# Kernel optimization log

Measured on AMD Instinct MI355X. Metric: run time of the kernel, lower is better.

## Reference

```python
import jax, jax.numpy as jnp
import numpy as np

D_MODEL = 1024
N_HEAD = 16
D_HEAD = D_MODEL // N_HEAD
B, S = 4, 2048


def setup_inputs() -> dict:
    key = jax.random.key(0)
    ks = jax.random.split(key, 9)
    s = 1.0 / np.sqrt(D_MODEL)
    inp = {"x": jax.random.normal(ks[0], (B, S, D_MODEL), dtype=jnp.float32)}
    for i, name in enumerate(["q", "k", "v", "o"]):
        inp[f"W{name}"] = jax.random.uniform(ks[1 + 2 * i], (D_MODEL, D_MODEL), jnp.float32, -s, s)
        inp[f"b{name}"] = jax.random.uniform(ks[2 + 2 * i], (D_MODEL,), jnp.float32, -s, s)
    return inp


def reference(x, Wq, bq, Wk, bk, Wv, bv, Wo, bo):
    b, sq, _ = x.shape
    skv = sq
    # projections (torch Linear: x @ W^T + b), reshape to (b, h, s, d)
    def proj(W, bias):
        return (x @ W.T + bias).reshape(b, sq, N_HEAD, D_HEAD).transpose(0, 2, 1, 3)
    q, k, v = proj(Wq, bq), proj(Wk, bk), proj(Wv, bv)
    scale = np.sqrt(D_HEAD).astype(np.float32)
    scores = jnp.einsum("bhqd,bhkd->bhqk", q, k) / scale
    causal_mask = jnp.triu(jnp.ones((sq, skv), dtype=bool), k=1)
    scores = jnp.where(causal_mask, -jnp.inf, scores)
    attn = jax.nn.softmax(scores, axis=-1)
    o = jnp.einsum("bhqk,bhkd->bhqd", attn, v)  # (b, h, sq, d_head)
    o = o.transpose(0, 2, 1, 3).reshape(b, sq, D_MODEL)
    return o @ Wo.T + bo
```

## Files before the change

kernel.cpp:

```cpp
#include <hip/hip_runtime.h>
#include <hip/hip_bf16.h>
#include <math.h>

#define S_LEN 2048
#define DMODEL 1024
#define NHEAD 16
#define DHEAD 64
#define BATCH 4
#define MROWS (BATCH * S_LEN)

typedef unsigned short u16;
typedef __attribute__((ext_vector_type(4))) unsigned short u16x4;
typedef __attribute__((ext_vector_type(2))) unsigned u32x2;
typedef __attribute__((ext_vector_type(8))) short bf16x8;
typedef __attribute__((ext_vector_type(4))) float f32x4;

#define GLDS16(g, l)                                              \
  __builtin_amdgcn_global_load_lds(                               \
      (const __attribute__((address_space(1))) void*)(g),         \
      (__attribute__((address_space(3))) void*)(l), 16, 0, 0)

__device__ __forceinline__ u16 f2bf(float f) {
  unsigned u = __float_as_uint(f);
  u += 0x7fff + ((u >> 16) & 1);
  return (u16)(u >> 16);
}

__device__ __forceinline__ float exp2v(float x) {
  float r;
  asm("v_exp_f32 %0, %1" : "=v"(r) : "v"(x));
  return r;
}

__device__ __forceinline__ f32x4 mfma16(bf16x8 a, bf16x8 b, f32x4 c) {
  return __builtin_amdgcn_mfma_f32_16x16x32_bf16(a, b, c, 0, 0, 0);
}

__global__ __launch_bounds__(256) void castk(const float* __restrict__ in,
                                             u16* __restrict__ out, int n) {
  int i = (blockIdx.x * 256 + threadIdx.x) * 4;
  if (i >= n) return;
  f32x4 v = *(const f32x4*)(in + i);
  u16 a0 = f2bf(v[0]), a1 = f2bf(v[1]), a2 = f2bf(v[2]), a3 = f2bf(v[3]);
  out[i + 0] = a0; out[i + 1] = a1; out[i + 2] = a2; out[i + 3] = a3;
}

__global__ __launch_bounds__(256) void castw(
    const float* __restrict__ i0, const float* __restrict__ i1,
    const float* __restrict__ i2, const float* __restrict__ i3,
    u16* __restrict__ o0, u16* __restrict__ o1,
    u16* __restrict__ o2, u16* __restrict__ o3) {
  const int m = blockIdx.y;
  const float* in = m == 0 ? i0 : (m == 1 ? i1 : (m == 2 ? i2 : i3));
  u16* out = m == 0 ? o0 : (m == 1 ? o1 : (m == 2 ? o2 : o3));
  int i = (blockIdx.x * 256 + threadIdx.x) * 4;
  f32x4 v = *(const f32x4*)(in + i);
  u16 a0 = f2bf(v[0]), a1 = f2bf(v[1]), a2 = f2bf(v[2]), a3 = f2bf(v[3]);
  out[i + 0] = a0; out[i + 1] = a1; out[i + 2] = a2; out[i + 3] = a3;
}

__global__ __launch_bounds__(256) void gemm_qkv(
    const u16* __restrict__ Xb,
    const u16* __restrict__ W0, const u16* __restrict__ W1, const u16* __restrict__ W2,
    const float* __restrict__ b0, const float* __restrict__ b1, const float* __restrict__ b2,
    u16* __restrict__ O0, u16* __restrict__ O1, u16* __restrict__ O2) {
  __shared__ u16 As[128 * 32];
  __shared__ u16 Bs[128 * 32];
  const int flat = blockIdx.x;
  const int xcd = flat & 7, idx = flat >> 3;
  const int ymt = xcd * 8 + idx / 24;
  const int rem = idx % 24;
  const int xnt = rem & 7;
  const int z = rem >> 3;
  const u16* Wm = z == 0 ? W0 : (z == 1 ? W1 : W2);
  const float* bias = z == 0 ? b0 : (z == 1 ? b1 : b2);
  u16* Out = z == 0 ? O0 : (z == 1 ? O1 : O2);
  const float qs = (z == 0) ? 0.18033688011112042f : 1.0f;
  const int tid = threadIdx.x;
  const int wave = tid >> 6, lane = tid & 63, g = lane >> 4, c = lane & 15;
  const int wm = wave >> 1, wn = wave & 1;
  const int bm0 = ymt * 128, bn0 = xnt * 128;
  const int o = tid * 16;
  const int row = o >> 6;
  const int kp8 = ((o >> 4) & 3) * 8;
  char* lA = (char*)As + wave * 1024;
  char* lB = (char*)Bs + wave * 1024;

  f32x4 acc[4][4];
#pragma unroll
  for (int m = 0; m < 4; ++m)
#pragma unroll
    for (int n = 0; n < 4; ++n) acc[m][n] = (f32x4){0.f, 0.f, 0.f, 0.f};

  for (int k0 = 0; k0 < DMODEL; k0 += 32) {
    __syncthreads();
    GLDS16(Xb + (size_t)(bm0 + row) * DMODEL + k0 + kp8, lA);
    GLDS16(Xb + (size_t)(bm0 + row + 64) * DMODEL + k0 + kp8, lA + 4096);
    GLDS16(Wm + (size_t)(bn0 + row) * DMODEL + k0 + kp8, lB);
    GLDS16(Wm + (size_t)(bn0 + row + 64) * DMODEL + k0 + kp8, lB + 4096);
    __syncthreads();
    bf16x8 af[4], bfr[4];
#pragma unroll
    for (int m = 0; m < 4; ++m)
      af[m] = *(const bf16x8*)(As + (wm * 64 + m * 16 + c) * 32 + g * 8);
#pragma unroll
    for (int n = 0; n < 4; ++n)
      bfr[n] = *(const bf16x8*)(Bs + (wn * 64 + n * 16 + c) * 32 + g * 8);
#pragma unroll
    for (int m = 0; m < 4; ++m)
#pragma unroll
      for (int n = 0; n < 4; ++n)
        acc[m][n] = mfma16(af[m], bfr[n], acc[m][n]);
  }
  if (z < 2) {
#pragma unroll
    for (int n = 0; n < 4; ++n) {
      const int coln = bn0 + wn * 64 + n * 16 + c;
      const float bn_ = bias[coln];
      const int h = coln >> 6, d = coln & 63;
#pragma unroll
      for (int m = 0; m < 4; ++m) {
#pragma unroll
        for (int r = 0; r < 4; ++r) {
          const int rowm = bm0 + wm * 64 + m * 16 + g * 4 + r;
          const int b_ = rowm >> 11, s_ = rowm & 2047;
          Out[(((size_t)(b_ * NHEAD + h) * S_LEN + s_) << 6) + d] =
              f2bf((acc[m][n][r] + bn_) * qs);
        }
      }
    }
  } else {
#pragma unroll
    for (int n = 0; n < 4; ++n) {
      const int coln = bn0 + wn * 64 + n * 16 + c;
      const float bn_ = bias[coln];
      const int h = coln >> 6, d = coln & 63;
#pragma unroll
      for (int m = 0; m < 4; ++m) {
        const int row0 = bm0 + wm * 64 + m * 16 + g * 4;
        const int b_ = row0 >> 11, s_ = row0 & 2047;
        u16x4 pk;
#pragma unroll
        for (int r = 0; r < 4; ++r) pk[r] = f2bf(acc[m][n][r] + bn_);
        *(u16x4*)(Out + ((size_t)(b_ * NHEAD + h) * DHEAD + d) * S_LEN + s_) = pk;
      }
    }
  }
}

__global__ __launch_bounds__(256) void gemm_out(
    const u16* __restrict__ Ab, const u16* __restrict__ Wm,
    const float* __restrict__ bias, float* __restrict__ Out) {
  __shared__ u16 As[128 * 32];
  __shared__ u16 Bs[128 * 32];
  const int flat = blockIdx.x;
  const int xcd = flat & 7, idx = flat >> 3;
  const int ymt = xcd * 8 + (idx >> 3);
  const int xnt = idx & 7;
  const int tid = threadIdx.x;
  const int wave = tid >> 6, lane = tid & 63, g = lane >> 4, c = lane & 15;
  const int wm = wave >> 1, wn = wave & 1;
  const int bm0 = ymt * 128, bn0 = xnt * 128;
  const int o = tid * 16;
  const int row = o >> 6;
  const int kp8 = ((o >> 4) & 3) * 8;
  char* lA = (char*)As + wave * 1024;
  char* lB = (char*)Bs + wave * 1024;

  f32x4 acc[4][4];
#pragma unroll
  for (int m = 0; m < 4; ++m)
#pragma unroll
    for (int n = 0; n < 4; ++n) acc[m][n] = (f32x4){0.f, 0.f, 0.f, 0.f};

  for (int k0 = 0; k0 < DMODEL; k0 += 32) {
    __syncthreads();
    GLDS16(Ab + (size_t)(bm0 + row) * DMODEL + k0 + kp8, lA);
    GLDS16(Ab + (size_t)(bm0 + row + 64) * DMODEL + k0 + kp8, lA + 4096);
    GLDS16(Wm + (size_t)(bn0 + row) * DMODEL + k0 + kp8, lB);
    GLDS16(Wm + (size_t)(bn0 + row + 64) * DMODEL + k0 + kp8, lB + 4096);
    __syncthreads();
    bf16x8 af[4], bfr[4];
#pragma unroll
    for (int m = 0; m < 4; ++m)
      af[m] = *(const bf16x8*)(As + (wm * 64 + m * 16 + c) * 32 + g * 8);
#pragma unroll
    for (int n = 0; n < 4; ++n)
      bfr[n] = *(const bf16x8*)(Bs + (wn * 64 + n * 16 + c) * 32 + g * 8);
#pragma unroll
    for (int m = 0; m < 4; ++m)
#pragma unroll
      for (int n = 0; n < 4; ++n)
        acc[m][n] = mfma16(af[m], bfr[n], acc[m][n]);
  }
#pragma unroll
  for (int n = 0; n < 4; ++n) {
    const int coln = bn0 + wn * 64 + n * 16 + c;
    const float bn_ = bias[coln];
#pragma unroll
    for (int m = 0; m < 4; ++m) {
#pragma unroll
      for (int r = 0; r < 4; ++r) {
        const int rowm = bm0 + wm * 64 + m * 16 + g * 4 + r;
        Out[(size_t)rowm * DMODEL + coln] = acc[m][n][r] + bn_;
      }
    }
  }
}

__global__ __launch_bounds__(256) void attn_fwd(const u16* __restrict__ Qb,
                                                const u16* __restrict__ Kb,
                                                const u16* __restrict__ VTb,
                                                u16* __restrict__ AOb) {
  __shared__ u16 Kt[64 * 64];
  __shared__ u16 Vt[64 * 64];
  __shared__ unsigned Pl[4][16 * 36];
  const int tid = threadIdx.x;
  const int w = tid >> 6, lane = tid & 63, g = lane >> 4, c = lane & 15;
  const int flat = blockIdx.x;
  const int wg = (flat & 7) * 128 + (flat >> 3);
  const int bh = wg >> 4;
  const int pr = wg & 15;
  const size_t base = (size_t)bh * (S_LEN * DHEAD);
  const int b_ = bh >> 4, h = bh & 15;
  const int ci0 = w * 64 + lane;

#pragma unroll
  for (int pass = 0; pass < 2; ++pass) {
    const int qt = pass ? pr : (31 - pr);
    const int qb = qt * 64;
    const int q = qb + w * 16 + c;
    const bf16x8 qf0 = *(const bf16x8*)(Qb + base + (size_t)q * 64 + g * 8);
    const bf16x8 qf1 = *(const bf16x8*)(Qb + base + (size_t)q * 64 + 32 + g * 8);

    f32x4 oacc[4];
#pragma unroll
    for (int dt = 0; dt < 4; ++dt) oacc[dt] = (f32x4){0.f, 0.f, 0.f, 0.f};
    float m = -30000.f, l = 0.f;

    const int nt = qt + 1;
    for (int kt = 0; kt < nt; ++kt) {
      const int kv0 = kt * 64;
      __syncthreads();
#pragma unroll
      for (int call = 0; call < 2; ++call) {
        const int ci = call * 256 + ci0;
        const int row = ci >> 3;
        const int colg = (ci & 7) ^ (row & 7);
        GLDS16(Kb + base + (size_t)(kv0 + row) * 64 + colg * 8,
               (char*)Kt + (call * 256 + w * 64) * 16);
        GLDS16(VTb + base + (size_t)row * S_LEN + kv0 + colg * 8,
               (char*)Vt + (call * 256 + w * 64) * 16);
      }
      __syncthreads();

      f32x4 s[4];
#pragma unroll
      for (int t = 0; t < 4; ++t) {
        const int krow = t * 16 + c;
        const char* kbase = (const char*)Kt + krow * 128;
        bf16x8 kf0 = *(const bf16x8*)(kbase + ((g ^ (krow & 7)) * 16));
        bf16x8 kf1 = *(const bf16x8*)(kbase + (((4 + g) ^ (krow & 7)) * 16));
        f32x4 zacc = (f32x4){0.f, 0.f, 0.f, 0.f};
        zacc = mfma16(kf0, qf0, zacc);
        zacc = mfma16(kf1, qf1, zacc);
        s[t] = zacc;
      }
      if (kt == nt - 1) {
#pragma unroll
        for (int t = 0; t < 4; ++t)
#pragma unroll
          for (int r = 0; r < 4; ++r)
            if (kv0 + t * 16 + 4 * g + r > q) s[t][r] = -30000.f;
      }
      const float a0 = fmaxf(fmaxf(s[0][0], s[0][1]), s[0][2]);
      const float a1 = fmaxf(fmaxf(s[0][3], s[1][0]), s[1][1]);
      const float a2 = fmaxf(fmaxf(s[1][2], s[1][3]), s[2][0]);
      const float a3 = fmaxf(fmaxf(s[2][1], s[2][2]), s[2][3]);
      const float a4 = fmaxf(fmaxf(s[3][0], s[3][1]), s[3][2]);
      float pm = fmaxf(fmaxf(fmaxf(a0, a1), a2), fmaxf(fmaxf(a3, a4), s[3][3]));
      pm = fmaxf(pm, __shfl_xor(pm, 16));
      pm = fmaxf(pm, __shfl_xor(pm, 32));
      if (__any(pm > m + 8.0f)) {
        const float mn = fmaxf(m, pm);
        const float sc = exp2v(m - mn);
        l *= sc;
#pragma unroll
        for (int dt = 0; dt < 4; ++dt) oacc[dt] *= sc;
        m = mn;
      }
      float rs = 0.f;
#pragma unroll
      for (int t = 0; t < 4; ++t) {
        const float p0 = exp2v(s[t][0] - m), p1 = exp2v(s[t][1] - m);
        const float p2 = exp2v(s[t][2] - m), p3 = exp2v(s[t][3] - m);
        rs += (p0 + p1) + (p2 + p3);
        const unsigned b0 = __float_as_uint(p0) + 0x8000u;
        const unsigned b1 = __float_as_uint(p1) + 0x8000u;
        const unsigned b2 = __float_as_uint(p2) + 0x8000u;
        const unsigned b3 = __float_as_uint(p3) + 0x8000u;
        u32x2 pk2;
        pk2[0] = __builtin_amdgcn_perm(b1, b0, 0x07060302u);
        pk2[1] = __builtin_amdgcn_perm(b3, b2, 0x07060302u);
        *(u32x2*)&Pl[w][c * 36 + t * 8 + g * 2] = pk2;
      }
      rs += __shfl_xor(rs, 16);
      rs += __shfl_xor(rs, 32);
      l += rs;

#pragma unroll
      for (int kk = 0; kk < 2; ++kk) {
        const bf16x8 pb = *(const bf16x8*)&Pl[w][c * 36 + kk * 16 + g * 4];
#pragma unroll
        for (int dt = 0; dt < 4; ++dt) {
          const int vrow = dt * 16 + c;
          const bf16x8 vf = *(const bf16x8*)((const char*)Vt + vrow * 128 +
                                             (((kk * 4 + g) ^ (vrow & 7)) * 16));
          oacc[dt] = mfma16(vf, pb, oacc[dt]);
        }
      }
    }
    const float inv = 1.0f / l;
    const size_t rowbase = ((size_t)(b_ * S_LEN + q) * DMODEL) + h * 64;
#pragma unroll
    for (int dt = 0; dt < 4; ++dt) {
      u16x4 pk4;
#pragma unroll
      for (int r = 0; r < 4; ++r) pk4[r] = f2bf(oacc[dt][r] * inv);
      *(u16x4*)(AOb + rowbase + dt * 16 + 4 * g) = pk4;
    }
  }
}

extern "C" void kernel_launch(void* const* d_in, const int* in_sizes, int n_in,
                              void* d_out, int out_size, void* d_ws, size_t ws_size,
                              hipStream_t stream) {
  const float* x  = (const float*)d_in[0];
  const float* Wq = (const float*)d_in[1];
  const float* bq = (const float*)d_in[2];
  const float* Wk = (const float*)d_in[3];
  const float* bk = (const float*)d_in[4];
  const float* Wv = (const float*)d_in[5];
  const float* bv = (const float*)d_in[6];
  const float* Wo = (const float*)d_in[7];
  const float* bo = (const float*)d_in[8];
  float* out = (float*)d_out;
  char* ws = (char*)d_ws;

  const size_t MB = 1024 * 1024;
  u16* xb  = (u16*)(ws);
  u16* Wqb = (u16*)(ws + 16 * MB);
  u16* Wkb = (u16*)(ws + 18 * MB);
  u16* Wvb = (u16*)(ws + 20 * MB);
  u16* Wob = (u16*)(ws + 22 * MB);
  u16* Qb  = (u16*)(ws + 24 * MB);
  u16* Kb  = (u16*)(ws + 40 * MB);
  u16* VTb = (u16*)(ws + 56 * MB);
  u16* AOb = (u16*)(ws + 72 * MB);

  castk<<<8192, 256, 0, stream>>>(x, xb, MROWS * DMODEL);
  castw<<<dim3(1024, 4), 256, 0, stream>>>(Wq, Wk, Wv, Wo, Wqb, Wkb, Wvb, Wob);

  gemm_qkv<<<1536, 256, 0, stream>>>(
      xb, Wqb, Wkb, Wvb, bq, bk, bv, Qb, Kb, VTb);

  attn_fwd<<<1024, 256, 0, stream>>>(Qb, Kb, VTb, AOb);

  gemm_out<<<512, 256, 0, stream>>>(AOb, Wob, bo, out);
}
```

Measured before the change: 187.3 us.

## Double GEMM K-tile to 64 with XOR-swizzled LDS layout

Both projection GEMMs now stage a 64-wide K slice per iteration instead of 32, halving the number of barrier pairs per tile. The global-to-LDS loads pick which 16-byte chunk each row fetches so that the chunk index is XORed with the row's low bits, and the fragment reads apply the same XOR so they hit different LDS banks. The goals are less synchronisation overhead and fewer LDS bank conflicts on the MFMA operand reads. The cost is doubled LDS per block, which may reduce occupancy.

```diff
diff --git a/kernel.cpp b/kernel.cpp
--- a/kernel.cpp
+++ b/kernel.cpp
@@ -64,8 +64,8 @@
     const u16* __restrict__ W0, const u16* __restrict__ W1, const u16* __restrict__ W2,
     const float* __restrict__ b0, const float* __restrict__ b1, const float* __restrict__ b2,
     u16* __restrict__ O0, u16* __restrict__ O1, u16* __restrict__ O2) {
-  __shared__ u16 As[128 * 32];
-  __shared__ u16 Bs[128 * 32];
+  __shared__ u16 As[128 * 64];
+  __shared__ u16 Bs[128 * 64];
   const int flat = blockIdx.x;
   const int xcd = flat & 7, idx = flat >> 3;
   const int ymt = xcd * 8 + idx / 24;
@@ -80,11 +80,6 @@
   const int wave = tid >> 6, lane = tid & 63, g = lane >> 4, c = lane & 15;
   const int wm = wave >> 1, wn = wave & 1;
   const int bm0 = ymt * 128, bn0 = xnt * 128;
-  const int o = tid * 16;
-  const int row = o >> 6;
-  const int kp8 = ((o >> 4) & 3) * 8;
-  char* lA = (char*)As + wave * 1024;
-  char* lB = (char*)Bs + wave * 1024;
 
   f32x4 acc[4][4];
 #pragma unroll
@@ -92,25 +87,40 @@
 #pragma unroll
     for (int n = 0; n < 4; ++n) acc[m][n] = (f32x4){0.f, 0.f, 0.f, 0.f};
 
-  for (int k0 = 0; k0 < DMODEL; k0 += 32) {
+  for (int k0 = 0; k0 < DMODEL; k0 += 64) {
     __syncthreads();
-    GLDS16(Xb + (size_t)(bm0 + row) * DMODEL + k0 + kp8, lA);
-    GLDS16(Xb + (size_t)(bm0 + row + 64) * DMODEL + k0 + kp8, lA + 4096);
-    GLDS16(Wm + (size_t)(bn0 + row) * DMODEL + k0 + kp8, lB);
-    GLDS16(Wm + (size_t)(bn0 + row + 64) * DMODEL + k0 + kp8, lB + 4096);
+#pragma unroll
+    for (int cc = 0; cc < 4; ++cc) {
+      const int ci = cc * 256 + tid;
+      const int row = ci >> 3, ch = ci & 7;
+      const int sc = ((ch ^ (row & 7)) << 3);
+      GLDS16(Xb + (size_t)(bm0 + row) * DMODEL + k0 + sc,
+             (char*)As + (cc * 256 + wave * 64) * 16);
+      GLDS16(Wm + (size_t)(bn0 + row) * DMODEL + k0 + sc,
+             (char*)Bs + (cc * 256 + wave * 64) * 16);
+    }
     __syncthreads();
-    bf16x8 af[4], bfr[4];
-#pragma unroll
-    for (int m = 0; m < 4; ++m)
-      af[m] = *(const bf16x8*)(As + (wm * 64 + m * 16 + c) * 32 + g * 8);
-#pragma unroll
-    for (int n = 0; n < 4; ++n)
-      bfr[n] = *(const bf16x8*)(Bs + (wn * 64 + n * 16 + c) * 32 + g * 8);
-#pragma unroll
-    for (int m = 0; m < 4; ++m)
-#pragma unroll
-      for (int n = 0; n < 4; ++n)
-        acc[m][n] = mfma16(af[m], bfr[n], acc[m][n]);
+#pragma unroll
+    for (int ks = 0; ks < 2; ++ks) {
+      bf16x8 af[4], bfr[4];
+#pragma unroll
+      for (int m = 0; m < 4; ++m) {
+        const int arow = wm * 64 + m * 16 + c;
+        af[m] = *(const bf16x8*)((const char*)As + arow * 128 +
+                                 (((ks * 4 + g) ^ (arow & 7)) << 4));
+      }
+#pragma unroll
+      for (int n = 0; n < 4; ++n) {
+        const int brow = wn * 64 + n * 16 + c;
+        bfr[n] = *(const bf16x8*)((const char*)Bs + brow * 128 +
+                                  (((ks * 4 + g) ^ (brow & 7)) << 4));
+      }
+#pragma unroll
+      for (int m = 0; m < 4; ++m)
+#pragma unroll
+        for (int n = 0; n < 4; ++n)
+          acc[m][n] = mfma16(af[m], bfr[n], acc[m][n]);
+    }
   }
   if (z < 2) {
 #pragma unroll
@@ -151,8 +161,8 @@
 __global__ __launch_bounds__(256) void gemm_out(
     const u16* __restrict__ Ab, const u16* __restrict__ Wm,
     const float* __restrict__ bias, float* __restrict__ Out) {
-  __shared__ u16 As[128 * 32];
-  __shared__ u16 Bs[128 * 32];
+  __shared__ u16 As[128 * 64];
+  __shared__ u16 Bs[128 * 64];
   const int flat = blockIdx.x;
   const int xcd = flat & 7, idx = flat >> 3;
   const int ymt = xcd * 8 + (idx >> 3);
@@ -161,11 +171,6 @@
   const int wave = tid >> 6, lane = tid & 63, g = lane >> 4, c = lane & 15;
   const int wm = wave >> 1, wn = wave & 1;
   const int bm0 = ymt * 128, bn0 = xnt * 128;
-  const int o = tid * 16;
-  const int row = o >> 6;
-  const int kp8 = ((o >> 4) & 3) * 8;
-  char* lA = (char*)As + wave * 1024;
-  char* lB = (char*)Bs + wave * 1024;
 
   f32x4 acc[4][4];
 #pragma unroll
@@ -173,25 +178,40 @@
 #pragma unroll
     for (int n = 0; n < 4; ++n) acc[m][n] = (f32x4){0.f, 0.f, 0.f, 0.f};
 
-  for (int k0 = 0; k0 < DMODEL; k0 += 32) {
+  for (int k0 = 0; k0 < DMODEL; k0 += 64) {
     __syncthreads();
-    GLDS16(Ab + (size_t)(bm0 + row) * DMODEL + k0 + kp8, lA);
-    GLDS16(Ab + (size_t)(bm0 + row + 64) * DMODEL + k0 + kp8, lA + 4096);
-    GLDS16(Wm + (size_t)(bn0 + row) * DMODEL + k0 + kp8, lB);
-    GLDS16(Wm + (size_t)(bn0 + row + 64) * DMODEL + k0 + kp8, lB + 4096);
+#pragma unroll
+    for (int cc = 0; cc < 4; ++cc) {
+      const int ci = cc * 256 + tid;
+      const int row = ci >> 3, ch = ci & 7;
+      const int sc = ((ch ^ (row & 7)) << 3);
+      GLDS16(Ab + (size_t)(bm0 + row) * DMODEL + k0 + sc,
+             (char*)As + (cc * 256 + wave * 64) * 16);
+      GLDS16(Wm + (size_t)(bn0 + row) * DMODEL + k0 + sc,
+             (char*)Bs + (cc * 256 + wave * 64) * 16);
+    }
     __syncthreads();
-    bf16x8 af[4], bfr[4];
-#pragma unroll
-    for (int m = 0; m < 4; ++m)
-      af[m] = *(const bf16x8*)(As + (wm * 64 + m * 16 + c) * 32 + g * 8);
-#pragma unroll
-    for (int n = 0; n < 4; ++n)
-      bfr[n] = *(const bf16x8*)(Bs + (wn * 64 + n * 16 + c) * 32 + g * 8);
-#pragma unroll
-    for (int m = 0; m < 4; ++m)
-#pragma unroll
-      for (int n = 0; n < 4; ++n)
-        acc[m][n] = mfma16(af[m], bfr[n], acc[m][n]);
+#pragma unroll
+    for (int ks = 0; ks < 2; ++ks) {
+      bf16x8 af[4], bfr[4];
+#pragma unroll
+      for (int m = 0; m < 4; ++m) {
+        const int arow = wm * 64 + m * 16 + c;
+        af[m] = *(const bf16x8*)((const char*)As + arow * 128 +
+                                 (((ks * 4 + g) ^ (arow & 7)) << 4));
+      }
+#pragma unroll
+      for (int n = 0; n < 4; ++n) {
+        const int brow = wn * 64 + n * 16 + c;
+        bfr[n] = *(const bf16x8*)((const char*)Bs + brow * 128 +
+                                  (((ks * 4 + g) ^ (brow & 7)) << 4));
+      }
+#pragma unroll
+      for (int m = 0; m < 4; ++m)
+#pragma unroll
+        for (int n = 0; n < 4; ++n)
+          acc[m][n] = mfma16(af[m], bfr[n], acc[m][n]);
+    }
   }
 #pragma unroll
   for (int n = 0; n < 4; ++n) {
```

Result: faster. 179.0 us (-4.4%).
